# Kernel optimization log

Hardware: AMD Instinct MI355X
Metric: run time of the kernel (lower is better)

The kernel has to match this reference:

```python
import jax, jax.numpy as jnp
import numpy as np

QK_SCALE = 10.0  # fixed scale used with qk_norm (x-transformers/zeta default)
NEG_INF = -1e9


def layernorm(x, g, b, eps=1e-5):
    mu = jnp.mean(x, axis=-1, keepdims=True)
    var = jnp.var(x, axis=-1, keepdims=True)
    return (x - mu) * jax.lax.rsqrt(var + eps) * g + b


def l2norm(x, eps=1e-12):
    return x / jnp.sqrt(jnp.sum(x * x, axis=-1, keepdims=True) + eps)


def setup_inputs() -> dict:
    key = jax.random.key(0)
    ks = jax.random.split(key, 10)
    B, S, D, H, DH, E, FF = 2, 1024, 1024, 16, 64, 8, 4096
    sd = lambda fan: 1.0 / np.sqrt(fan)
    return {
        'x': jax.random.normal(ks[0], (B, S, D), jnp.float32),
        'ln_g': jnp.ones((D,), jnp.float32),
        'ln_b': jnp.zeros((D,), jnp.float32),
        'Wq': jax.random.normal(ks[1], (D, H * DH), jnp.float32) * sd(D),
        'Wk': jax.random.normal(ks[2], (D, H * DH), jnp.float32) * sd(D),
        'Wv': jax.random.normal(ks[3], (D, H * DH), jnp.float32) * sd(D),
        'q_scale': jnp.ones((H, 1, DH), jnp.float32),
        'k_scale': jnp.ones((H, 1, DH), jnp.float32),
        'Wo': jax.random.normal(ks[4], (H * DH, D), jnp.float32) * sd(H * DH),
        'gate_w': jax.random.normal(ks[5], (D, E), jnp.float32) * sd(D),
        'gate_b': jnp.zeros((E,), jnp.float32),
        'w1': jax.random.normal(ks[6], (E, D, FF), jnp.float32) * sd(D),
        'b1': jnp.zeros((E, FF), jnp.float32),
        'w2': jax.random.normal(ks[7], (E, FF, D), jnp.float32) * sd(FF),
        'b2': jnp.zeros((E, D), jnp.float32),
    }


def reference(x, ln_g, ln_b, Wq, Wk, Wv, q_scale, k_scale, Wo,
              gate_w, gate_b, w1, b1, w2, b2):
    B, S, D = x.shape
    H = q_scale.shape[0]
    DH = q_scale.shape[-1]

    # pre-attention LayerNorm (shared params)
    h = layernorm(x, ln_g, ln_b)

    # qk-normed causal multi-head attention
    q = (h @ Wq).reshape(B, S, H, DH).transpose(0, 2, 1, 3)  # b h s d
    k = (h @ Wk).reshape(B, S, H, DH).transpose(0, 2, 1, 3)
    v = (h @ Wv).reshape(B, S, H, DH).transpose(0, 2, 1, 3)
    q = l2norm(q) * q_scale
    k = l2norm(k) * k_scale
    logits = jnp.einsum('bhid,bhjd->bhij', q, k) * QK_SCALE
    causal = jnp.tril(jnp.ones((S, S), bool))
    logits = jnp.where(causal, logits, NEG_INF)
    attn = jax.nn.softmax(logits, axis=-1)
    out = jnp.einsum('bhij,bhjd->bhid', attn, v)
    out = out.transpose(0, 2, 1, 3).reshape(B, S, H * DH) @ Wo

    # mid LayerNorm (same shared params)
    h = layernorm(out, ln_g, ln_b)

    # SimpleMoE: softmax gate, dense combine over all experts
    gate = jax.nn.softmax(h @ gate_w + gate_b, axis=-1)  # b s e
    hid = jax.nn.gelu(jnp.einsum('bsd,edf->bsef', h, w1) + b1)  # b s e ff
    exp_out = jnp.einsum('bsef,efd->bsed', hid, w2) + b2  # b s e d
    moe = jnp.einsum('bse,bsed->bsd', gate, exp_out)

    # final LayerNorm (same shared params)
    return layernorm(moe, ln_g, ln_b)
```

## Files before the change

### kernel.cpp

```cpp
#include <hip/hip_runtime.h>

typedef unsigned short u16;
typedef float f32x4 __attribute__((ext_vector_type(4)));
typedef short short8 __attribute__((ext_vector_type(8)));

#define QK_SCALE_F 10.0f

#define GLD_LDS(g, l) __builtin_amdgcn_global_load_lds( \
    (const __attribute__((address_space(1))) unsigned int*)(g), \
    (__attribute__((address_space(3))) unsigned int*)(l), 16, 0, 0)

__device__ __forceinline__ u16 f2b(float f) {
  union { float f; unsigned u; } c; c.f = f;
  return (u16)((c.u + 0x7fffu + ((c.u >> 16) & 1u)) >> 16);
}

__device__ __forceinline__ float wred_sum(float v) {
#pragma unroll
  for (int m = 32; m > 0; m >>= 1) v += __shfl_xor(v, m, 64);
  return v;
}
__device__ __forceinline__ float wred_max(float v) {
#pragma unroll
  for (int m = 32; m > 0; m >>= 1) v = fmaxf(v, __shfl_xor(v, m, 64));
  return v;
}

#define BM 128
#define BN 128
#define BKK 64

template<int EPI>
__global__ __launch_bounds__(256)
void gemm_bt(const u16* __restrict__ A, const u16* __restrict__ B, void* __restrict__ Cv,
             int M, int N, int K, int lda, int ldb, int ldc,
             long zA, long zB, long zC,
             const float* __restrict__ P1, long zP1, const float* __restrict__ P2,
             int causal) {
  int z = blockIdx.z;
  int row0 = blockIdx.y * BM;
  int col0 = blockIdx.x * BN;
  if (causal && col0 > row0 + (BM - 1)) return;
  A += zA * z; B += zB * z;
  int tid = threadIdx.x;
  int wave = tid >> 6, lane = tid & 63;
  int wm = wave >> 1, wn = wave & 1;

  __shared__ __align__(16) u16 lA[BM * BKK];
  __shared__ __align__(16) u16 lB[BN * BKK];

  f32x4 acc[4][4];
  f32x4 zf = {0.f, 0.f, 0.f, 0.f};
#pragma unroll
  for (int i = 0; i < 4; i++)
#pragma unroll
    for (int j = 0; j < 4; j++) acc[i][j] = zf;

  int l3 = lane >> 3;
  int scol = ((lane & 7) ^ l3) << 3;
  long aoff[4], boff[4];
  int cbase[4];
#pragma unroll
  for (int i = 0; i < 4; i++) {
    int c = (wave << 2) + i;
    int r = (c << 3) + l3;
    aoff[i] = (long)(row0 + r) * lda + scol;
    boff[i] = (long)(col0 + r) * ldb + scol;
    cbase[i] = c << 10;
  }

  for (int k0 = 0; k0 < K; k0 += BKK) {
    __syncthreads();
#pragma unroll
    for (int i = 0; i < 4; i++) {
      GLD_LDS(A + aoff[i] + k0, (char*)lA + cbase[i]);
      GLD_LDS(B + boff[i] + k0, (char*)lB + cbase[i]);
    }
    __syncthreads();
#pragma unroll
    for (int kk = 0; kk < 2; kk++) {
      short8 af[4], bfr[4];
      int cb = (kk << 6) | ((lane >> 4) << 4);
#pragma unroll
      for (int mi = 0; mi < 4; mi++) {
        int R = (wm << 6) + (mi << 4) + (lane & 15);
        af[mi] = *(const short8*)((const char*)lA + ((R << 7) | (cb ^ ((R & 7) << 4))));
      }
#pragma unroll
      for (int nj = 0; nj < 4; nj++) {
        int R = (wn << 6) + (nj << 4) + (lane & 15);
        bfr[nj] = *(const short8*)((const char*)lB + ((R << 7) | (cb ^ ((R & 7) << 4))));
      }
#pragma unroll
      for (int mi = 0; mi < 4; mi++)
#pragma unroll
        for (int nj = 0; nj < 4; nj++)
          acc[mi][nj] = __builtin_amdgcn_mfma_f32_16x16x32_bf16(af[mi], bfr[nj], acc[mi][nj], 0, 0, 0);
    }
  }

#pragma unroll
  for (int mi = 0; mi < 4; mi++) {
#pragma unroll
    for (int nj = 0; nj < 4; nj++) {
#pragma unroll
      for (int rr = 0; rr < 4; rr++) {
        int row = row0 + (wm << 6) + (mi << 4) + ((lane >> 4) << 2) + rr;
        int col = col0 + (wn << 6) + (nj << 4) + (lane & 15);
        if (col < N) {
          float v = acc[mi][nj][rr];
          long cidx = zC * z + (long)row * ldc + col;
          if (EPI == 0) {
            ((float*)Cv)[cidx] = v;
          } else if (EPI == 2) {
            float t = v + P1[zP1 * z + col];
            float gl = 0.5f * t * (1.f + tanhf(0.7978845608f * (t + 0.044715f * t * t * t)));
            ((u16*)Cv)[cidx] = f2b(gl * P2[((long)row << 3) + z]);
          } else if (EPI == 4) {
            atomicAdd(&((float*)Cv)[cidx], v);
          }
        }
      }
    }
  }
}

__global__ __launch_bounds__(256)
void transpose_cast(const float* __restrict__ src, u16* __restrict__ dst,
                    int R, int C, long sz, long dz) {
  int z = blockIdx.z;
  src += sz * z; dst += dz * z;
  __shared__ float t[32][33];
  int c0 = blockIdx.x * 32, r0 = blockIdx.y * 32;
  int tx = threadIdx.x & 31, ty = threadIdx.x >> 5;
#pragma unroll
  for (int j = 0; j < 4; j++) {
    int r = ty + j * 8;
    t[r][tx] = src[(long)(r0 + r) * C + c0 + tx];
  }
  __syncthreads();
#pragma unroll
  for (int j = 0; j < 4; j++) {
    int r = ty + j * 8;
    dst[(long)(c0 + r) * R + r0 + tx] = f2b(t[tx][r]);
  }
}

__global__ __launch_bounds__(256)
void ln_kernel(const float* __restrict__ x, const float* __restrict__ g,
               const float* __restrict__ b, float* __restrict__ yf, u16* __restrict__ yb) {
  int tid = threadIdx.x;
  long base = (long)blockIdx.x << 10;
  float4 v = *(const float4*)&x[base + tid * 4];
  float s = v.x + v.y + v.z + v.w;
  float q = v.x * v.x + v.y * v.y + v.z * v.z + v.w * v.w;
  s = wred_sum(s); q = wred_sum(q);
  __shared__ float2 red[4];
  int wave = tid >> 6, lane = tid & 63;
  if (lane == 0) red[wave] = make_float2(s, q);
  __syncthreads();
  float S1 = red[0].x + red[1].x + red[2].x + red[3].x;
  float S2 = red[0].y + red[1].y + red[2].y + red[3].y;
  float mu = S1 * (1.f / 1024.f);
  float var = S2 * (1.f / 1024.f) - mu * mu;
  float rs = rsqrtf(var + 1e-5f);
  float4 gv = *(const float4*)&g[tid * 4];
  float4 bv = *(const float4*)&b[tid * 4];
  float4 o;
  o.x = (v.x - mu) * rs * gv.x + bv.x;
  o.y = (v.y - mu) * rs * gv.y + bv.y;
  o.z = (v.z - mu) * rs * gv.z + bv.z;
  o.w = (v.w - mu) * rs * gv.w + bv.w;
  if (yf) *(float4*)&yf[base + tid * 4] = o;
  if (yb) {
    ushort4 ob; ob.x = f2b(o.x); ob.y = f2b(o.y); ob.z = f2b(o.z); ob.w = f2b(o.w);
    *(ushort4*)&yb[base + tid * 4] = ob;
  }
}

__global__ __launch_bounds__(256)
void l2norm_kernel(const float* __restrict__ src, const float* __restrict__ scale,
                   u16* __restrict__ dst, int ld, int off) {
  int r = blockIdx.x * 4 + (threadIdx.x >> 6);
  int lane = threadIdx.x & 63;
  float v = src[(long)(r >> 4) * ld + off + ((r & 15) << 6) + lane];
  float ss = v * v;
#pragma unroll
  for (int m = 32; m > 0; m >>= 1) ss += __shfl_xor(ss, m, 64);
  int h = r & 15, sIdx = (r >> 4) & 1023, b = r >> 14;
  float o = v * rsqrtf(ss + 1e-12f) * scale[(h << 6) + lane];
  dst[((((long)(b * 16 + h)) << 10) + sIdx) * 64 + lane] = f2b(o);
}

__global__ __launch_bounds__(256)
void v_transpose(const float* __restrict__ vf, u16* __restrict__ vT) {
  int z = blockIdx.x, b = z >> 4, h = z & 15, s0 = blockIdx.y * 16;
  __shared__ u16 t[64][17];
  int si = threadIdx.x >> 6, d = threadIdx.x & 63;
#pragma unroll
  for (int j = 0; j < 4; j++) {
    int sl = j * 4 + si;
    t[d][sl] = f2b(vf[((long)(b << 10) + (s0 + sl)) * 3072 + 2048 + (h << 6) + d]);
  }
  __syncthreads();
  int d2 = threadIdx.x >> 2, sj = threadIdx.x & 3;
#pragma unroll
  for (int j = 0; j < 4; j++) {
    int sl = j * 4 + sj;
    vT[((long)(z * 128 + d2) << 10) + s0 + sl] = t[d2][sl];
  }
}

__global__ __launch_bounds__(256)
void softmax_kernel(const float* __restrict__ logits, u16* __restrict__ P) {
  int i = blockIdx.x, z = blockIdx.y, tid = threadIdx.x;
  long base = ((long)z << 20) + ((long)i << 10);
  int len = i + 1;
  float lv[4];
  float mx = -1e30f;
  int cnt = 0;
  for (int j = tid; j < len; j += 256) { float l = logits[base + j] * QK_SCALE_F; lv[cnt++] = l; mx = fmaxf(mx, l); }
  mx = wred_max(mx);
  __shared__ float red[4];
  int wave = tid >> 6, lane = tid & 63;
  if (lane == 0) red[wave] = mx;
  __syncthreads();
  mx = fmaxf(fmaxf(red[0], red[1]), fmaxf(red[2], red[3]));
  float s = 0.f;
  for (int c = 0; c < cnt; c++) { lv[c] = __expf(lv[c] - mx); s += lv[c]; }
  s = wred_sum(s);
  __syncthreads();
  if (lane == 0) red[wave] = s;
  __syncthreads();
  s = red[0] + red[1] + red[2] + red[3];
  float inv = 1.f / s;
  cnt = 0;
  for (int j = tid; j < len; j += 256) P[base + j] = f2b(lv[cnt++] * inv);
  for (int j = tid; j < 1024; j += 256) if (j >= len) P[base + j] = 0;
}

__global__ __launch_bounds__(256)
void attn_cat_kernel(const float* __restrict__ pv, u16* __restrict__ acat) {
  int blk = blockIdx.x; int b = blk >> 10, i = blk & 1023;
#pragma unroll
  for (int j = 0; j < 4; ++j) {
    int col = threadIdx.x + j * 256;
    int h = col >> 6, d = col & 63;
    float v = pv[(((long)(b * 16 + h)) << 16) + (i << 6) + d];
    acat[((long)blk << 10) + col] = f2b(v);
  }
}

__global__ __launch_bounds__(256)
void gate_kernel(const float* __restrict__ h2, const float* __restrict__ gw,
                 const float* __restrict__ gb, float* __restrict__ gate) {
  int row = blockIdx.x, tid = threadIdx.x;
  const float* hr = h2 + ((long)row << 10);
  float acc[8];
#pragma unroll
  for (int e = 0; e < 8; e++) acc[e] = 0.f;
  for (int d = tid; d < 1024; d += 256) {
    float hv = hr[d];
    const float4* wp = (const float4*)&gw[d * 8];
    float4 w0 = wp[0], w1v = wp[1];
    acc[0] += hv * w0.x;  acc[1] += hv * w0.y;  acc[2] += hv * w0.z;  acc[3] += hv * w0.w;
    acc[4] += hv * w1v.x; acc[5] += hv * w1v.y; acc[6] += hv * w1v.z; acc[7] += hv * w1v.w;
  }
  __shared__ float red[8][4];
  int wave = tid >> 6, lane = tid & 63;
#pragma unroll
  for (int e = 0; e < 8; e++) { float v = wred_sum(acc[e]); if (lane == 0) red[e][wave] = v; }
  __syncthreads();
  if (tid == 0) {
    float l[8]; float mx = -1e30f;
    for (int e = 0; e < 8; e++) { l[e] = red[e][0] + red[e][1] + red[e][2] + red[e][3] + gb[e]; mx = fmaxf(mx, l[e]); }
    float s = 0.f;
    for (int e = 0; e < 8; e++) { l[e] = __expf(l[e] - mx); s += l[e]; }
    float inv = 1.f / s;
    for (int e = 0; e < 8; e++) gate[row * 8 + e] = l[e] * inv;
  }
}

__global__ __launch_bounds__(256)
void bias_moe_kernel(const float* __restrict__ gate, const float* __restrict__ b2, float* __restrict__ moe) {
  int row = blockIdx.x, tid = threadIdx.x;
  __shared__ float gs[8];
  if (tid < 8) gs[tid] = gate[row * 8 + tid];
  __syncthreads();
  for (int col = tid; col < 1024; col += 256) {
    float s = 0.f;
#pragma unroll
    for (int e = 0; e < 8; e++) s += gs[e] * b2[(e << 10) + col];
    moe[((long)row << 10) + col] = s;
  }
}

extern "C" void kernel_launch(void* const* d_in, const int* in_sizes, int n_in,
                              void* d_out, int out_size, void* d_ws, size_t ws_size,
                              hipStream_t stream) {
  const float* x   = (const float*)d_in[0];
  const float* lng = (const float*)d_in[1];
  const float* lnb = (const float*)d_in[2];
  const float* Wq  = (const float*)d_in[3];
  const float* Wk  = (const float*)d_in[4];
  const float* Wv  = (const float*)d_in[5];
  const float* qs  = (const float*)d_in[6];
  const float* ks  = (const float*)d_in[7];
  const float* Wo  = (const float*)d_in[8];
  const float* gw  = (const float*)d_in[9];
  const float* gb  = (const float*)d_in[10];
  const float* w1  = (const float*)d_in[11];
  const float* b1  = (const float*)d_in[12];
  const float* w2  = (const float*)d_in[13];
  const float* b2  = (const float*)d_in[14];
  float* out = (float*)d_out;

  char* base = (char*)d_ws;
  size_t off = 0;
  auto alloc = [&](size_t bytes) { void* p = base + off; off = (off + bytes + 255) & ~(size_t)255; return p; };

  u16*   W1T  = (u16*)alloc(8l * 1024 * 4096 * 2);
  u16*   W2T  = (u16*)alloc(1024l * 32768 * 2);
  u16*   WQKVT= (u16*)alloc(3072l * 1024 * 2);
  u16*   WOT  = (u16*)alloc(1024l * 1024 * 2);
  u16*   HB   = (u16*)alloc(2048l * 1024 * 2);
  float* QKVF = (float*)alloc(2048l * 3072 * 4);
  u16*   QN   = (u16*)alloc(2048l * 1024 * 2);
  u16*   KN   = (u16*)alloc(2048l * 1024 * 2);
  u16*   VT   = (u16*)alloc(32l * 128 * 1024 * 2);
  float* LOG  = (float*)alloc(32l * 1024 * 1024 * 4);
  u16*   P    = (u16*)alloc(32l * 1024 * 1024 * 2);
  float* PV   = (float*)alloc(32l * 1024 * 64 * 4);
  u16*   ACAT = (u16*)alloc(2048l * 1024 * 2);
  float* APROJ= (float*)alloc(2048l * 1024 * 4);
  float* H2F  = (float*)alloc(2048l * 1024 * 4);
  u16*   H2B  = (u16*)alloc(2048l * 1024 * 2);
  float* GATE = (float*)alloc(2048l * 8 * 4);
  float* MOE  = (float*)alloc(2048l * 1024 * 4);
  u16*   HID  = (u16*)LOG;

  if (off > ws_size) return;

  dim3 blk(256);

  transpose_cast<<<dim3(32, 32, 1), blk, 0, stream>>>(Wq, WQKVT, 1024, 1024, 0, 0);
  transpose_cast<<<dim3(32, 32, 1), blk, 0, stream>>>(Wk, WQKVT + 1024l * 1024, 1024, 1024, 0, 0);
  transpose_cast<<<dim3(32, 32, 1), blk, 0, stream>>>(Wv, WQKVT + 2048l * 1024, 1024, 1024, 0, 0);
  transpose_cast<<<dim3(32, 32, 1), blk, 0, stream>>>(Wo, WOT, 1024, 1024, 0, 0);
  transpose_cast<<<dim3(128, 32, 8), blk, 0, stream>>>(w1, W1T, 1024, 4096, 1024l * 4096, 4096l * 1024);
  transpose_cast<<<dim3(32, 1024, 1), blk, 0, stream>>>(w2, W2T, 32768, 1024, 0, 0);

  ln_kernel<<<2048, blk, 0, stream>>>(x, lng, lnb, nullptr, HB);

  gemm_bt<0><<<dim3(24, 16, 1), blk, 0, stream>>>(HB, WQKVT, QKVF, 2048, 3072, 1024, 1024, 1024, 3072,
                                                  0, 0, 0, nullptr, 0, nullptr, 0);

  l2norm_kernel<<<8192, blk, 0, stream>>>(QKVF, qs, QN, 3072, 0);
  l2norm_kernel<<<8192, blk, 0, stream>>>(QKVF, ks, KN, 3072, 1024);
  v_transpose<<<dim3(32, 64, 1), blk, 0, stream>>>(QKVF, VT);

  gemm_bt<0><<<dim3(8, 8, 32), blk, 0, stream>>>(QN, KN, LOG, 1024, 1024, 64, 64, 64, 1024,
                                                 65536, 65536, 1048576, nullptr, 0, nullptr, 1);
  softmax_kernel<<<dim3(1024, 32, 1), blk, 0, stream>>>(LOG, P);
  gemm_bt<0><<<dim3(1, 8, 32), blk, 0, stream>>>(P, VT, PV, 1024, 64, 1024, 1024, 1024, 64,
                                                 1048576, 131072, 65536, nullptr, 0, nullptr, 0);
  attn_cat_kernel<<<2048, blk, 0, stream>>>(PV, ACAT);

  gemm_bt<0><<<dim3(8, 16, 1), blk, 0, stream>>>(ACAT, WOT, APROJ, 2048, 1024, 1024, 1024, 1024, 1024,
                                                 0, 0, 0, nullptr, 0, nullptr, 0);
  ln_kernel<<<2048, blk, 0, stream>>>(APROJ, lng, lnb, H2F, H2B);

  gate_kernel<<<2048, blk, 0, stream>>>(H2F, gw, gb, GATE);
  gemm_bt<2><<<dim3(32, 16, 8), blk, 0, stream>>>(H2B, W1T, HID, 2048, 4096, 1024, 1024, 1024, 32768,
                                                  0, 4096l * 1024, 4096, b1, 4096, GATE, 0);
  bias_moe_kernel<<<2048, blk, 0, stream>>>(GATE, b2, MOE);
  gemm_bt<4><<<dim3(8, 16, 8), blk, 0, stream>>>(HID, W2T, MOE, 2048, 1024, 4096, 32768, 32768, 1024,
                                                 4096, 4096, 0, nullptr, 0, nullptr, 0);

  ln_kernel<<<2048, blk, 0, stream>>>(MOE, lng, lnb, out, nullptr);
}
```

Measured before the change: 1.053 ms.

## Double-buffer GEMM LDS, use exp-based GELU, replace atomic MoE reduction with split-K buffer

```diff
diff --git a/kernel.cpp b/kernel.cpp
--- a/kernel.cpp
+++ b/kernel.cpp
@@ -46,8 +46,8 @@
   int wave = tid >> 6, lane = tid & 63;
   int wm = wave >> 1, wn = wave & 1;
 
-  __shared__ __align__(16) u16 lA[BM * BKK];
-  __shared__ __align__(16) u16 lB[BN * BKK];
+  __shared__ __align__(16) u16 lA[2][BM * BKK];
+  __shared__ __align__(16) u16 lB[2][BN * BKK];
 
   f32x4 acc[4][4];
   f32x4 zf = {0.f, 0.f, 0.f, 0.f};
@@ -69,14 +69,22 @@
     cbase[i] = c << 10;
   }
 
-  for (int k0 = 0; k0 < K; k0 += BKK) {
+  auto stage = [&](int buf, int k0) {
+#pragma unroll
+    for (int i = 0; i < 4; i++) {
+      GLD_LDS(A + aoff[i] + k0, (char*)lA[buf] + cbase[i]);
+      GLD_LDS(B + boff[i] + k0, (char*)lB[buf] + cbase[i]);
+    }
+  };
+
+  int nt = K / BKK;
+  stage(0, 0);
+  int cur = 0;
+  for (int t = 0; t < nt; ++t) {
     __syncthreads();
-#pragma unroll
-    for (int i = 0; i < 4; i++) {
-      GLD_LDS(A + aoff[i] + k0, (char*)lA + cbase[i]);
-      GLD_LDS(B + boff[i] + k0, (char*)lB + cbase[i]);
-    }
-    __syncthreads();
+    if (t + 1 < nt) stage(cur ^ 1, (t + 1) * BKK);
+    const char* pA = (const char*)lA[cur];
+    const char* pB = (const char*)lB[cur];
 #pragma unroll
     for (int kk = 0; kk < 2; kk++) {
       short8 af[4], bfr[4];
@@ -84,12 +92,12 @@
 #pragma unroll
       for (int mi = 0; mi < 4; mi++) {
         int R = (wm << 6) + (mi << 4) + (lane & 15);
-        af[mi] = *(const short8*)((const char*)lA + ((R << 7) | (cb ^ ((R & 7) << 4))));
+        af[mi] = *(const short8*)(pA + ((R << 7) | (cb ^ ((R & 7) << 4))));
       }
 #pragma unroll
       for (int nj = 0; nj < 4; nj++) {
         int R = (wn << 6) + (nj << 4) + (lane & 15);
-        bfr[nj] = *(const short8*)((const char*)lB + ((R << 7) | (cb ^ ((R & 7) << 4))));
+        bfr[nj] = *(const short8*)(pB + ((R << 7) | (cb ^ ((R & 7) << 4))));
       }
 #pragma unroll
       for (int mi = 0; mi < 4; mi++)
@@ -97,6 +105,7 @@
         for (int nj = 0; nj < 4; nj++)
           acc[mi][nj] = __builtin_amdgcn_mfma_f32_16x16x32_bf16(af[mi], bfr[nj], acc[mi][nj], 0, 0, 0);
     }
+    cur ^= 1;
   }
 
 #pragma unroll
@@ -114,10 +123,9 @@
             ((float*)Cv)[cidx] = v;
           } else if (EPI == 2) {
             float t = v + P1[zP1 * z + col];
-            float gl = 0.5f * t * (1.f + tanhf(0.7978845608f * (t + 0.044715f * t * t * t)));
+            float zz = 1.5957691216f * (t + 0.044715f * t * t * t);
+            float gl = t / (1.f + __expf(-zz));
             ((u16*)Cv)[cidx] = f2b(gl * P2[((long)row << 3) + z]);
-          } else if (EPI == 4) {
-            atomicAdd(&((float*)Cv)[cidx], v);
           }
         }
       }
@@ -179,6 +187,50 @@
 }
 
 __global__ __launch_bounds__(256)
+void ln_reduce8(const float* __restrict__ sl, const float* __restrict__ gate,
+                const float* __restrict__ b2, const float* __restrict__ g,
+                const float* __restrict__ b, float* __restrict__ out) {
+  int row = blockIdx.x, tid = threadIdx.x;
+  __shared__ float gs[8];
+  if (tid < 8) gs[tid] = gate[(row << 3) + tid];
+  __syncthreads();
+  long rbase = (long)row << 10;
+  int col = tid << 2;
+  float4 a = {0.f, 0.f, 0.f, 0.f};
+#pragma unroll
+  for (int s = 0; s < 8; s++) {
+    float4 v = *(const float4*)&sl[(long)s * (2048l * 1024) + rbase + col];
+    a.x += v.x; a.y += v.y; a.z += v.z; a.w += v.w;
+  }
+#pragma unroll
+  for (int e = 0; e < 8; e++) {
+    float4 bv = *(const float4*)&b2[(e << 10) + col];
+    float ge = gs[e];
+    a.x += ge * bv.x; a.y += ge * bv.y; a.z += ge * bv.z; a.w += ge * bv.w;
+  }
+  float s1 = a.x + a.y + a.z + a.w;
+  float q = a.x * a.x + a.y * a.y + a.z * a.z + a.w * a.w;
+  s1 = wred_sum(s1); q = wred_sum(q);
+  __shared__ float2 red[4];
+  int wave = tid >> 6, lane = tid & 63;
+  if (lane == 0) red[wave] = make_float2(s1, q);
+  __syncthreads();
+  float S1 = red[0].x + red[1].x + red[2].x + red[3].x;
+  float S2 = red[0].y + red[1].y + red[2].y + red[3].y;
+  float mu = S1 * (1.f / 1024.f);
+  float var = S2 * (1.f / 1024.f) - mu * mu;
+  float rs = rsqrtf(var + 1e-5f);
+  float4 gv = *(const float4*)&g[col];
+  float4 bv = *(const float4*)&b[col];
+  float4 o;
+  o.x = (a.x - mu) * rs * gv.x + bv.x;
+  o.y = (a.y - mu) * rs * gv.y + bv.y;
+  o.z = (a.z - mu) * rs * gv.z + bv.z;
+  o.w = (a.w - mu) * rs * gv.w + bv.w;
+  *(float4*)&out[rbase + col] = o;
+}
+
+__global__ __launch_bounds__(256)
 void l2norm_kernel(const float* __restrict__ src, const float* __restrict__ scale,
                    u16* __restrict__ dst, int ld, int off) {
   int r = blockIdx.x * 4 + (threadIdx.x >> 6);
@@ -278,20 +330,6 @@
     for (int e = 0; e < 8; e++) { l[e] = __expf(l[e] - mx); s += l[e]; }
     float inv = 1.f / s;
     for (int e = 0; e < 8; e++) gate[row * 8 + e] = l[e] * inv;
-  }
-}
-
-__global__ __launch_bounds__(256)
-void bias_moe_kernel(const float* __restrict__ gate, const float* __restrict__ b2, float* __restrict__ moe) {
-  int row = blockIdx.x, tid = threadIdx.x;
-  __shared__ float gs[8];
-  if (tid < 8) gs[tid] = gate[row * 8 + tid];
-  __syncthreads();
-  for (int col = tid; col < 1024; col += 256) {
-    float s = 0.f;
-#pragma unroll
-    for (int e = 0; e < 8; e++) s += gs[e] * b2[(e << 10) + col];
-    moe[((long)row << 10) + col] = s;
   }
 }
 
@@ -336,8 +374,8 @@
   float* H2F  = (float*)alloc(2048l * 1024 * 4);
   u16*   H2B  = (u16*)alloc(2048l * 1024 * 2);
   float* GATE = (float*)alloc(2048l * 8 * 4);
-  float* MOE  = (float*)alloc(2048l * 1024 * 4);
   u16*   HID  = (u16*)LOG;
+  float* MOE8 = (float*)P;
 
   if (off > ws_size) return;
 
@@ -373,9 +411,8 @@
   gate_kernel<<<2048, blk, 0, stream>>>(H2F, gw, gb, GATE);
   gemm_bt<2><<<dim3(32, 16, 8), blk, 0, stream>>>(H2B, W1T, HID, 2048, 4096, 1024, 1024, 1024, 32768,
                                                   0, 4096l * 1024, 4096, b1, 4096, GATE, 0);
-  bias_moe_kernel<<<2048, blk, 0, stream>>>(GATE, b2, MOE);
-  gemm_bt<4><<<dim3(8, 16, 8), blk, 0, stream>>>(HID, W2T, MOE, 2048, 1024, 4096, 32768, 32768, 1024,
-                                                 4096, 4096, 0, nullptr, 0, nullptr, 0);
-
-  ln_kernel<<<2048, blk, 0, stream>>>(MOE, lng, lnb, out, nullptr);
-}
+  gemm_bt<0><<<dim3(8, 16, 8), blk, 0, stream>>>(HID, W2T, MOE8, 2048, 1024, 4096, 32768, 32768, 1024,
+                                                 4096, 4096, 2048l * 1024, nullptr, 0, nullptr, 0);
+
+  ln_reduce8<<<2048, blk, 0, stream>>>(MOE8, GATE, b2, lng, lnb, out);
+}
```

Result: faster. 1.012 ms (-3.9%).
